# Optimization experiments

Hardware: AMD Instinct MI355X
Metric: run time of the kernel (lower is better)

The kernel has to match this reference:

```python
import jax, jax.numpy as jnp
import numpy as np

B, HP, WP = 4, 32, 32
T = HP * WP
C = 768            # n_embd
NH = 24            # n_head
HS = C // NH       # head_size == HEAD_SIZE == 32
E = HS             # TIME_MIX_EXTRA_DIM = HEAD_SIZE
D = 64             # TIME_DECAY_DIM


def setup_inputs() -> dict:
    key = jax.random.key(0)
    ks = jax.random.split(key, 24)
    small = lambda k, sh: jax.random.uniform(k, sh, jnp.float32, -1e-4, 1e-4)
    inp = {
        "x": jax.random.normal(ks[0], (B, T, C), jnp.float32),
        "time_maa_x": jax.random.uniform(ks[1], (1, 1, C), jnp.float32),
        "time_maa_w": jax.random.uniform(ks[2], (1, 1, C), jnp.float32),
        "time_maa_k": jax.random.uniform(ks[3], (1, 1, C), jnp.float32),
        "time_maa_v": jax.random.uniform(ks[4], (1, 1, C), jnp.float32),
        "time_maa_r": jax.random.uniform(ks[5], (1, 1, C), jnp.float32),
        "time_maa_g": jax.random.uniform(ks[6], (1, 1, C), jnp.float32),
        "time_maa_w1": small(ks[7], (C, 5 * E)),
        "time_maa_w2": small(ks[8], (5, E, C)),
        "time_decay": jnp.linspace(-6.0, -1.0, C, dtype=jnp.float32).reshape(1, 1, C),
        "time_decay_w1": small(ks[9], (C, D)),
        "time_decay_w2": small(ks[10], (D, C)),
        "time_faaaa": jax.random.uniform(ks[11], (NH, HS), jnp.float32, -0.1, 0.6),
        "W_r": jax.random.normal(ks[12], (C, C), jnp.float32) * 0.02,
        "W_k": jax.random.normal(ks[13], (C, C), jnp.float32) * 0.02,
        "W_v": jax.random.normal(ks[14], (C, C), jnp.float32) * 0.02,
        "W_g": jax.random.normal(ks[15], (C, C), jnp.float32) * 0.02,
        "W_o": jax.random.normal(ks[16], (C, C), jnp.float32) * 0.02,
        "ln_w": jnp.ones((C,), jnp.float32),
        "ln_b": jnp.zeros((C,), jnp.float32),
        "Hp": HP,
        "Wp": WP,
    }
    return inp


def q_shift(x, H, W):
    """groups_q_shift with K=1, gamma=1/4: quarter-channel 4-direction spatial shift, zero-padded."""
    Bs, Ts, Cs = x.shape
    g = x.reshape(Bs, H, W, Cs)
    c4 = Cs // 4
    a, b, c, d = g[..., :c4], g[..., c4:2 * c4], g[..., 2 * c4:3 * c4], g[..., 3 * c4:]
    a = jnp.pad(a[:, :, :-1], ((0, 0), (0, 0), (1, 0), (0, 0)))  # shift +W (right)
    b = jnp.pad(b[:, :, 1:], ((0, 0), (0, 0), (0, 1), (0, 0)))   # shift -W (left)
    c = jnp.pad(c[:, :-1], ((0, 0), (1, 0), (0, 0), (0, 0)))     # shift +H (down)
    d = jnp.pad(d[:, 1:], ((0, 0), (0, 1), (0, 0), (0, 0)))      # shift -H (up)
    return jnp.concatenate([a, b, c, d], axis=-1).reshape(Bs, Ts, Cs)


def wkv6(r, k, v, w, u):
    """RWKV6 WKV scan. r,k,v,w: (B,T,C); u: (NH,HS). decay = exp(-exp(w))."""
    Bs, Ts, Cs = r.shape
    rh = r.reshape(Bs, Ts, NH, HS)
    kh = k.reshape(Bs, Ts, NH, HS)
    vh = v.reshape(Bs, Ts, NH, HS)
    dh = jnp.exp(-jnp.exp(w)).reshape(Bs, Ts, NH, HS)

    def step(s, ins):
        rt, kt, vt, dt = ins                                   # each (B,NH,HS)
        kv = kt[..., :, None] * vt[..., None, :]               # (B,NH,HS,HS)
        y = jnp.einsum('bhj,bhji->bhi', rt, s + u[None, :, :, None] * kv)
        s = dt[..., :, None] * s + kv
        return s, y

    xs = (rh.transpose(1, 0, 2, 3), kh.transpose(1, 0, 2, 3),
          vh.transpose(1, 0, 2, 3), dh.transpose(1, 0, 2, 3))
    s0 = jnp.zeros((Bs, NH, HS, HS), r.dtype)
    _, ys = jax.lax.scan(step, s0, xs)                          # (T,B,NH,HS)
    return ys.transpose(1, 0, 2, 3).reshape(Bs, Ts, Cs)


def reference(x, time_maa_x, time_maa_w, time_maa_k, time_maa_v, time_maa_r,
              time_maa_g, time_maa_w1, time_maa_w2, time_decay, time_decay_w1,
              time_decay_w2, time_faaaa, W_r, W_k, W_v, W_g, W_o, ln_w, ln_b,
              Hp, Wp):
    Bs, Ts, Cs = x.shape
    xx = q_shift(x, Hp, Wp) - x                                 # token shift delta
    xxx = x + xx * time_maa_x
    xxx = jnp.tanh(xxx @ time_maa_w1).reshape(Bs, Ts, 5, E)
    mix = jnp.einsum('btke,kec->kbtc', xxx, time_maa_w2)        # (5,B,T,C)
    mw, mk, mv, mr, mg = mix[0], mix[1], mix[2], mix[3], mix[4]

    xw = x + xx * (time_maa_w + mw)
    xk = x + xx * (time_maa_k + mk)
    xv = x + xx * (time_maa_v + mv)
    xr = x + xx * (time_maa_r + mr)
    xg = x + xx * (time_maa_g + mg)

    r = xr @ W_r
    k = xk @ W_k
    v = xv @ W_v
    g = jax.nn.silu(xg @ W_g)

    ww = jnp.tanh(xw @ time_decay_w1) @ time_decay_w2
    w = time_decay + ww                                         # data-dependent log-decay

    y = wkv6(r, k, v, w, time_faaaa)

    # ln_x (LayerNorm over channels)
    mu = y.mean(-1, keepdims=True)
    var = ((y - mu) ** 2).mean(-1, keepdims=True)
    yn = (y - mu) / jnp.sqrt(var + 1e-5) * ln_w + ln_b

    return (yn * g) @ W_o
```

## Files before the change

### kernel.cpp

```cpp
#include <hip/hip_runtime.h>
#include <math.h>

#define BB   4
#define TT   1024
#define CC   768
#define NH_  24
#define HS_  32

static constexpr size_t SZ = (size_t)BB * TT * CC;

typedef __attribute__((ext_vector_type(8))) __bf16 bf16x8;
typedef __attribute__((ext_vector_type(4))) float  f32x4;

__device__ __forceinline__ unsigned short f2bf(float f) {
    unsigned u = __float_as_uint(f);
    unsigned r = (u + 0x7FFFu + ((u >> 16) & 1u)) >> 16;
    return (unsigned short)r;
}
__device__ __forceinline__ float bf2f(unsigned short h) {
    return __uint_as_float(((unsigned)h) << 16);
}

struct TDesc { const float* src; unsigned short* dst; int R, C; };
struct TArgs { TDesc d[8]; };

__global__ __launch_bounds__(256) void transpose_cast(TArgs a)
{
    __shared__ float tile[32][33];
    TDesc t = a.d[blockIdx.z];
    const int tx0 = blockIdx.x * 32, ty0 = blockIdx.y * 32;
    if (tx0 >= t.C || ty0 >= t.R) return;
    const int tx = threadIdx.x & 31, ty = threadIdx.x >> 5;
    #pragma unroll
    for (int dy = 0; dy < 4; ++dy) {
        int rr = ty0 + ty + dy * 8, cc = tx0 + tx;
        tile[ty + dy * 8][tx] = (rr < t.R && cc < t.C) ? t.src[(size_t)rr * t.C + cc] : 0.f;
    }
    __syncthreads();
    #pragma unroll
    for (int dy = 0; dy < 4; ++dy) {
        int cc = tx0 + ty + dy * 8, rr = ty0 + tx;
        if (cc < t.C && rr < t.R)
            t.dst[(size_t)cc * t.R + rr] = f2bf(tile[tx][ty + dy * 8]);
    }
}

__global__ __launch_bounds__(192) void w2fill(const float* __restrict__ w2,
                                              unsigned short* __restrict__ W2t)
{
    const int n = blockIdx.x;
    const int e = threadIdx.x;
    if (e >= 160) return;
    const int kk = n / 768;
    const int c  = n - kk * 768;
    unsigned short val = 0;
    if ((e >> 5) == kk) val = f2bf(w2[(size_t)e * 768 + c]);
    W2t[(size_t)n * 160 + e] = val;
}

__global__ __launch_bounds__(256) void shift_kernel(
    const float* __restrict__ x, const float* __restrict__ maa_x,
    float* __restrict__ xxO, unsigned short* __restrict__ xxxO)
{
    const int tok = blockIdx.x;
    const int t   = tok & (TT - 1);
    const int hh  = t >> 5;
    const int wp  = t & 31;
    const int tid = threadIdx.x;
    const float* xrow = x + (size_t)tok * CC;
    for (int c = tid; c < CC; c += 256) {
        float xc = xrow[c];
        float sh;
        if (c < 192)      sh = (wp > 0)  ? xrow[c - CC]      : 0.f;
        else if (c < 384) sh = (wp < 31) ? xrow[c + CC]      : 0.f;
        else if (c < 576) sh = (hh > 0)  ? xrow[c - 32 * CC] : 0.f;
        else              sh = (hh < 31) ? xrow[c + 32 * CC] : 0.f;
        float xxv = sh - xc;
        size_t o = (size_t)tok * CC + c;
        xxO[o]  = xxv;
        xxxO[o] = f2bf(fmaf(xxv, maa_x[c], xc));
    }
}

template<int KDIM, class Epi>
__device__ __forceinline__ void gemm_core(const unsigned short* __restrict__ A,
                                          const unsigned short* __restrict__ W,
                                          int N, const Epi& epi)
{
    __shared__ __align__(16) unsigned short As[64][40];
    __shared__ __align__(16) unsigned short Bs[64][40];

    const int tid  = threadIdx.x;
    const int lane = tid & 63;
    const int wv   = tid >> 6;
    const int wm   = (wv >> 1) * 32, wn = (wv & 1) * 32;
    const int m0   = blockIdx.y * 64, n0 = blockIdx.x * 64;
    const int srow = tid >> 2, scb = (tid & 3) * 8;
    const int l15  = lane & 15, kb8 = (lane >> 4) * 8;

    f32x4 acc[2][2];
    #pragma unroll
    for (int a = 0; a < 2; ++a)
        #pragma unroll
        for (int b = 0; b < 2; ++b)
            #pragma unroll
            for (int e = 0; e < 4; ++e) acc[a][b][e] = 0.f;

    const unsigned short* aP = A + (size_t)(m0 + srow) * KDIM + scb;
    const unsigned short* bP = W + (size_t)(n0 + srow) * KDIM + scb;
    const bool bvalid = (n0 + srow) < N;

    for (int k0 = 0; k0 < KDIM; k0 += 32) {
        uint4 av = *(const uint4*)(aP + k0);
        uint4 bw = make_uint4(0u, 0u, 0u, 0u);
        if (bvalid) bw = *(const uint4*)(bP + k0);
        *(uint4*)&As[srow][scb] = av;
        *(uint4*)&Bs[srow][scb] = bw;
        __syncthreads();

        bf16x8 a0 = *(const bf16x8*)&As[wm + l15][kb8];
        bf16x8 a1 = *(const bf16x8*)&As[wm + 16 + l15][kb8];
        bf16x8 b0 = *(const bf16x8*)&Bs[wn + l15][kb8];
        bf16x8 b1 = *(const bf16x8*)&Bs[wn + 16 + l15][kb8];
        acc[0][0] = __builtin_amdgcn_mfma_f32_16x16x32_bf16(a0, b0, acc[0][0], 0, 0, 0);
        acc[0][1] = __builtin_amdgcn_mfma_f32_16x16x32_bf16(a0, b1, acc[0][1], 0, 0, 0);
        acc[1][0] = __builtin_amdgcn_mfma_f32_16x16x32_bf16(a1, b0, acc[1][0], 0, 0, 0);
        acc[1][1] = __builtin_amdgcn_mfma_f32_16x16x32_bf16(a1, b1, acc[1][1], 0, 0, 0);
        __syncthreads();
    }

    const int rb_ = m0 + wm + (lane >> 4) * 4;
    #pragma unroll
    for (int mi = 0; mi < 2; ++mi)
        #pragma unroll
        for (int ni = 0; ni < 2; ++ni) {
            int col = n0 + wn + ni * 16 + l15;
            if (col < N) {
                #pragma unroll
                for (int j = 0; j < 4; ++j)
                    epi(rb_ + mi * 16 + j, col, acc[mi][ni][j]);
            }
        }
}

struct EpiTanh {
    unsigned short* O; int ldo;
    __device__ void operator()(int r, int c, float v) const {
        O[(size_t)r * ldo + c] = f2bf(tanhf(v));
    }
};
struct EpiF32 {
    float* O;
    __device__ void operator()(int r, int c, float v) const {
        O[(size_t)r * 768 + c] = v;
    }
};
struct EpiDec {
    const float* td; float* O;
    __device__ void operator()(int r, int c, float v) const {
        O[(size_t)r * 768 + c] = expf(-expf(td[c] + v));
    }
};
struct EpiMix {
    const float* px; const float* pxx;
    const float* maa[5];
    unsigned short* outs[5];
    __device__ void operator()(int r, int c, float v) const {
        int kk = c / 768;
        int cc = c - kk * 768;
        size_t o = (size_t)r * 768 + cc;
        outs[kk][o] = f2bf(fmaf(pxx[o], maa[kk][cc] + v, px[o]));
    }
};
struct EpiRKVG {
    unsigned short* O; bool silu;
    __device__ void operator()(int r, int c, float v) const {
        if (silu) v = v / (1.f + expf(-v));
        O[(size_t)r * 768 + c] = f2bf(v);
    }
};

template<int KDIM, class Epi>
__global__ __launch_bounds__(256) void gemm_one(const unsigned short* __restrict__ A,
                                                const unsigned short* __restrict__ W,
                                                int N, Epi epi)
{
    gemm_core<KDIM>(A, W, N, epi);
}

struct QuadArgs {
    const unsigned short* A[4];
    const unsigned short* W[4];
    unsigned short* O[4];
};
__global__ __launch_bounds__(256) void gemm_quad768(QuadArgs q)
{
    const int z = blockIdx.z;
    EpiRKVG e{q.O[z], z == 3};
    gemm_core<768>(q.A[z], q.W[z], 768, e);
}

__global__ __launch_bounds__(256) void wkv_scan(
    const unsigned short* __restrict__ r, const unsigned short* __restrict__ k,
    const unsigned short* __restrict__ v, const float* __restrict__ dec,
    const float* __restrict__ u, float* __restrict__ y)
{
    __shared__ __align__(16) unsigned short rwL[64][40], kwL[64][40];
    __shared__ __align__(16) unsigned short vT0[32][40], vT1[32][40];
    __shared__ __align__(16) unsigned short rsL[64][40], ksL[64][40];
    __shared__ __align__(16) unsigned short ksT0[32][40], ksT1[32][40];
    __shared__ __align__(16) unsigned short PL0[64][40], PL1[64][40];
    __shared__ __align__(16) unsigned short STb[32][40];
    __shared__ float ST[32][32];
    __shared__ float AL[65][32];
    __shared__ float segprod[8][32];
    __shared__ float dpart[64][4];
    __shared__ float diagL[64];
    __shared__ float uL[32];

    const int bh = blockIdx.x;
    const int b = bh / NH_, h = bh % NH_;
    const int tid  = threadIdx.x;
    const int lane = tid & 63;
    const int wv   = tid >> 6;
    const int l15  = lane & 15;
    const int kb8  = (lane >> 4) * 8;
    const int rb4  = (lane >> 4) * 4;

    const size_t base0 = ((size_t)b * TT) * CC + (size_t)h * HS_;

    if (tid < 32) uL[tid] = u[h * HS_ + tid];
    for (int q = tid; q < 1024; q += 256) {
        ST[q >> 5][q & 31]  = 0.f;
        STb[q >> 5][q & 31] = 0;
    }
    __syncthreads();

    const int lrow = tid >> 2, lq = (tid & 3) * 8;
    const int cj = tid & 31, cseg = tid >> 5;

    for (int tc = 0; tc < TT; tc += 64) {
        {
            size_t gp = base0 + (size_t)(tc + lrow) * CC + lq;
            uint4 rv = *(const uint4*)(r + gp);
            uint4 kv = *(const uint4*)(k + gp);
            uint4 vv = *(const uint4*)(v + gp);
            *(uint4*)&rwL[lrow][lq] = rv;
            *(uint4*)&kwL[lrow][lq] = kv;
            const unsigned short* vp = (const unsigned short*)&vv;
            if (lrow < 32) {
                #pragma unroll
                for (int e = 0; e < 8; ++e) vT0[lq + e][lrow] = vp[e];
            } else {
                #pragma unroll
                for (int e = 0; e < 8; ++e) vT1[lq + e][lrow - 32] = vp[e];
            }
        }
        float dv[8];
        #pragma unroll
        for (int q = 0; q < 8; ++q)
            dv[q] = dec[base0 + (size_t)(tc + cseg * 8 + q) * CC + cj];
        {
            float lp = dv[0];
            #pragma unroll
            for (int q = 1; q < 8; ++q) lp *= dv[q];
            segprod[cseg][cj] = lp;
        }
        __syncthreads();

        {
            const int ptau = tid >> 2, pp = tid & 3;
            float acc = 0.f;
            #pragma unroll
            for (int e = 0; e < 8; ++e) {
                int j = pp * 8 + e;
                acc += bf2f(rwL[ptau][j]) * uL[j] * bf2f(kwL[ptau][j]);
            }
            dpart[ptau][pp] = acc;
        }
        {
            float pre = 1.f;
            #pragma unroll
            for (int s = 0; s < 7; ++s) if (s < cseg) pre *= segprod[s][cj];
            float run = pre;
            #pragma unroll
            for (int q = 0; q < 8; ++q) {
                AL[cseg * 8 + q][cj] = run;
                run *= dv[q];
            }
            if (cseg == 7) AL[64][cj] = run;
        }
        __syncthreads();

        if (tid < 64)
            diagL[tid] = dpart[tid][0] + dpart[tid][1] + dpart[tid][2] + dpart[tid][3];

        #pragma unroll
        for (int q = 0; q < 8; ++q) {
            int tau = cseg * 8 + q;
            float a  = AL[tau][cj];
            float ia = 1.f / AL[tau + 1][cj];
            unsigned short rs = f2bf(bf2f(rwL[tau][cj]) * a);
            unsigned short ks = f2bf(bf2f(kwL[tau][cj]) * ia);
            rsL[tau][cj] = rs;
            ksL[tau][cj] = ks;
            if (tau < 32) ksT0[cj][tau] = ks; else ksT1[cj][tau - 32] = ks;
        }
        __syncthreads();

        {
            const int wm = (wv >> 1) * 32, wn = (wv & 1) * 32;
            bf16x8 a0 = *(const bf16x8*)&rsL[wm + l15][kb8];
            bf16x8 a1 = *(const bf16x8*)&rsL[wm + 16 + l15][kb8];
            bf16x8 b0 = *(const bf16x8*)&ksL[wn + l15][kb8];
            bf16x8 b1 = *(const bf16x8*)&ksL[wn + 16 + l15][kb8];
            f32x4 qf[2][2];
            #pragma unroll
            for (int mi = 0; mi < 2; ++mi)
                #pragma unroll
                for (int ni = 0; ni < 2; ++ni)
                    #pragma unroll
                    for (int e = 0; e < 4; ++e) qf[mi][ni][e] = 0.f;
            qf[0][0] = __builtin_amdgcn_mfma_f32_16x16x32_bf16(a0, b0, qf[0][0], 0, 0, 0);
            qf[0][1] = __builtin_amdgcn_mfma_f32_16x16x32_bf16(a0, b1, qf[0][1], 0, 0, 0);
            qf[1][0] = __builtin_amdgcn_mfma_f32_16x16x32_bf16(a1, b0, qf[1][0], 0, 0, 0);
            qf[1][1] = __builtin_amdgcn_mfma_f32_16x16x32_bf16(a1, b1, qf[1][1], 0, 0, 0);
            #pragma unroll
            for (int mi = 0; mi < 2; ++mi)
                #pragma unroll
                for (int ni = 0; ni < 2; ++ni) {
                    const int col = wn + ni * 16 + l15;
                    #pragma unroll
                    for (int jj = 0; jj < 4; ++jj) {
                        const int row = wm + mi * 16 + rb4 + jj;
                        float val = (col < row) ? qf[mi][ni][jj]
                                  : ((col == row) ? diagL[row] : 0.f);
                        unsigned short bvv = f2bf(val);
                        if (col < 32) PL0[row][col] = bvv;
                        else          PL1[row][col - 32] = bvv;
                    }
                }
        }
        __syncthreads();

        {
            const int mr = wv * 16;
            bf16x8 pa0 = *(const bf16x8*)&PL0[mr + l15][kb8];
            bf16x8 pa1 = *(const bf16x8*)&PL1[mr + l15][kb8];
            bf16x8 ra  = *(const bf16x8*)&rsL[mr + l15][kb8];
            #pragma unroll
            for (int ni = 0; ni < 2; ++ni) {
                bf16x8 bv0 = *(const bf16x8*)&vT0[ni * 16 + l15][kb8];
                bf16x8 bv1 = *(const bf16x8*)&vT1[ni * 16 + l15][kb8];
                bf16x8 bs  = *(const bf16x8*)&STb[ni * 16 + l15][kb8];
                f32x4 acc;
                #pragma unroll
                for (int e = 0; e < 4; ++e) acc[e] = 0.f;
                acc = __builtin_amdgcn_mfma_f32_16x16x32_bf16(pa0, bv0, acc, 0, 0, 0);
                acc = __builtin_amdgcn_mfma_f32_16x16x32_bf16(pa1, bv1, acc, 0, 0, 0);
                acc = __builtin_amdgcn_mfma_f32_16x16x32_bf16(ra,  bs,  acc, 0, 0, 0);
                #pragma unroll
                for (int jj = 0; jj < 4; ++jj)
                    y[base0 + (size_t)(tc + mr + rb4 + jj) * CC + ni * 16 + l15] = acc[jj];
            }
        }
        __syncthreads();

        {
            const int mi = (wv >> 1) * 16, nj = (wv & 1) * 16;
            bf16x8 av0 = *(const bf16x8*)&vT0[mi + l15][kb8];
            bf16x8 av1 = *(const bf16x8*)&vT1[mi + l15][kb8];
            bf16x8 bk0 = *(const bf16x8*)&ksT0[nj + l15][kb8];
            bf16x8 bk1 = *(const bf16x8*)&ksT1[nj + l15][kb8];
            f32x4 acc;
            #pragma unroll
            for (int e = 0; e < 4; ++e) acc[e] = 0.f;
            acc = __builtin_amdgcn_mfma_f32_16x16x32_bf16(av0, bk0, acc, 0, 0, 0);
            acc = __builtin_amdgcn_mfma_f32_16x16x32_bf16(av1, bk1, acc, 0, 0, 0);
            const int j = nj + l15;
            const float D = AL[64][j];
            #pragma unroll
            for (int jj = 0; jj < 4; ++jj) {
                const int i = mi + rb4 + jj;
                float ns = D * (ST[i][j] + acc[jj]);
                ST[i][j]  = ns;
                STb[i][j] = f2bf(ns);
            }
        }
        __syncthreads();
    }
}

__global__ __launch_bounds__(256) void ln_gate(
    const float* __restrict__ y, const unsigned short* __restrict__ g,
    const float* __restrict__ lnw, const float* __restrict__ lnb,
    unsigned short* __restrict__ z)
{
    __shared__ float sy[CC];
    __shared__ float rbuf[8];
    __shared__ float stats[2];

    const int row = blockIdx.x, tid = threadIdx.x;
    const float* yr = y + (size_t)row * CC;

    float s1 = 0.f, s2 = 0.f;
    #pragma unroll
    for (int q = 0; q < 3; ++q) {
        int c = tid + q * 256;
        float vv = yr[c];
        sy[c] = vv;
        s1 += vv;
        s2 += vv * vv;
    }
    #pragma unroll
    for (int off = 32; off > 0; off >>= 1) {
        s1 += __shfl_down(s1, off);
        s2 += __shfl_down(s2, off);
    }
    const int wid = tid >> 6;
    if ((tid & 63) == 0) { rbuf[wid] = s1; rbuf[4 + wid] = s2; }
    __syncthreads();
    if (tid == 0) {
        float S1 = rbuf[0] + rbuf[1] + rbuf[2] + rbuf[3];
        float S2 = rbuf[4] + rbuf[5] + rbuf[6] + rbuf[7];
        float mu = S1 / (float)CC;
        float var = S2 / (float)CC - mu * mu;
        stats[0] = mu;
        stats[1] = rsqrtf(var + 1e-5f);
    }
    __syncthreads();
    const float mu = stats[0], rstd = stats[1];
    const unsigned short* gr = g + (size_t)row * CC;
    unsigned short* zr = z + (size_t)row * CC;
    #pragma unroll
    for (int q = 0; q < 3; ++q) {
        int c = tid + q * 256;
        zr[c] = f2bf(fmaf((sy[c] - mu) * rstd, lnw[c], lnb[c]) * bf2f(gr[c]));
    }
}

extern "C" void kernel_launch(void* const* d_in, const int* in_sizes, int n_in,
                              void* d_out, int out_size, void* d_ws, size_t ws_size,
                              hipStream_t stream)
{
    const float* x      = (const float*)d_in[0];
    const float* maa_x  = (const float*)d_in[1];
    const float* maa_w  = (const float*)d_in[2];
    const float* maa_k  = (const float*)d_in[3];
    const float* maa_v  = (const float*)d_in[4];
    const float* maa_r  = (const float*)d_in[5];
    const float* maa_g  = (const float*)d_in[6];
    const float* w1     = (const float*)d_in[7];
    const float* w2     = (const float*)d_in[8];
    const float* tdec   = (const float*)d_in[9];
    const float* tdw1   = (const float*)d_in[10];
    const float* tdw2   = (const float*)d_in[11];
    const float* faaaa  = (const float*)d_in[12];
    const float* Wr     = (const float*)d_in[13];
    const float* Wk     = (const float*)d_in[14];
    const float* Wv     = (const float*)d_in[15];
    const float* Wg     = (const float*)d_in[16];
    const float* Wo     = (const float*)d_in[17];
    const float* lnw    = (const float*)d_in[18];
    const float* lnb    = (const float*)d_in[19];

    char* base = (char*)d_ws;
    size_t off = 0;
    auto alloc = [&](size_t bytes) -> char* {
        char* p = base + off;
        off = (off + bytes + 255) & ~(size_t)255;
        return p;
    };

    float*          xx   = (float*)alloc(SZ * 4);
    float*          decb = (float*)alloc(SZ * 4);
    unsigned short* xxx  = (unsigned short*)alloc(SZ * 2);
    unsigned short* xw   = (unsigned short*)alloc(SZ * 2);
    unsigned short* xk   = (unsigned short*)alloc(SZ * 2);
    unsigned short* xv   = (unsigned short*)alloc(SZ * 2);
    unsigned short* xr   = (unsigned short*)alloc(SZ * 2);
    unsigned short* xg   = (unsigned short*)alloc(SZ * 2);
    unsigned short* rb   = (unsigned short*)alloc(SZ * 2);
    unsigned short* kb   = (unsigned short*)alloc(SZ * 2);
    unsigned short* vb   = (unsigned short*)alloc(SZ * 2);
    unsigned short* gb   = (unsigned short*)alloc(SZ * 2);
    unsigned short* t5   = (unsigned short*)alloc((size_t)4096 * 160 * 2);
    unsigned short* d1   = (unsigned short*)alloc((size_t)4096 * 64 * 2);
    unsigned short* w1t  = (unsigned short*)alloc((size_t)160 * 768 * 2);
    unsigned short* w2t  = (unsigned short*)alloc((size_t)3840 * 160 * 2);
    unsigned short* wrt  = (unsigned short*)alloc((size_t)768 * 768 * 2);
    unsigned short* wkt  = (unsigned short*)alloc((size_t)768 * 768 * 2);
    unsigned short* wvt  = (unsigned short*)alloc((size_t)768 * 768 * 2);
    unsigned short* wgt  = (unsigned short*)alloc((size_t)768 * 768 * 2);
    unsigned short* wot  = (unsigned short*)alloc((size_t)768 * 768 * 2);
    unsigned short* td1t = (unsigned short*)alloc((size_t)64 * 768 * 2);
    unsigned short* td2t = (unsigned short*)alloc((size_t)768 * 64 * 2);
    float*          y    = xx;
    unsigned short* z    = xxx;

    TArgs ta = {{
        { w1,   w1t,  768, 160 },
        { Wr,   wrt,  768, 768 },
        { Wk,   wkt,  768, 768 },
        { Wv,   wvt,  768, 768 },
        { Wg,   wgt,  768, 768 },
        { Wo,   wot,  768, 768 },
        { tdw1, td1t, 768, 64  },
        { tdw2, td2t, 64,  768 },
    }};
    transpose_cast<<<dim3(24, 24, 8), 256, 0, stream>>>(ta);
    w2fill<<<3840, 192, 0, stream>>>(w2, w2t);

    shift_kernel<<<BB * TT, 256, 0, stream>>>(x, maa_x, xx, xxx);

    gemm_one<768, EpiTanh><<<dim3(3, 64), 256, 0, stream>>>(xxx, w1t, 160, EpiTanh{t5, 160});

    EpiMix em{ x, xx,
               { maa_w, maa_k, maa_v, maa_r, maa_g },
               { xw, xk, xv, xr, xg } };
    gemm_one<160, EpiMix><<<dim3(60, 64), 256, 0, stream>>>(t5, w2t, 3840, em);

    gemm_one<768, EpiTanh><<<dim3(1, 64), 256, 0, stream>>>(xw, td1t, 64, EpiTanh{d1, 64});

    gemm_one<64, EpiDec><<<dim3(12, 64), 256, 0, stream>>>(d1, td2t, 768, EpiDec{tdec, decb});

    QuadArgs qa = {{ xr, xk, xv, xg }, { wrt, wkt, wvt, wgt }, { rb, kb, vb, gb }};
    gemm_quad768<<<dim3(12, 64, 4), 256, 0, stream>>>(qa);

    wkv_scan<<<BB * NH_, 256, 0, stream>>>(rb, kb, vb, decb, faaaa, y);

    ln_gate<<<BB * TT, 256, 0, stream>>>(y, gb, lnw, lnb, z);

    gemm_one<768, EpiF32><<<dim3(12, 64), 256, 0, stream>>>(z, wot, 768, EpiF32{(float*)d_out});
}
```

Baseline: 321.7 us.

## Split WKV scan into chunk-parallel local/carry/state-add kernels; use 128x128 GEMM tiles

The sequential per-head WKV scan, which used only 96 blocks, is split into three kernels. The first computes each 64-token chunk's intra-chunk output and chunk kv outer product in parallel (16 chunks × 96 heads). The second is a short serial carry of the state across chunks, and the third adds the r·state contribution per chunk. Separately, the mix, RKVG quad and output GEMMs move to a new 128x128 tile core with more MFMA work per LDS load. This adds extra kernel launches and global round trips for the intermediates, reuses scratch buffers, and cuts block counts for the GEMMs.

After: 302.7 us. 1.06x faster.

```diff
diff --git a/kernel.cpp b/kernel.cpp
--- a/kernel.cpp
+++ b/kernel.cpp
@@ -6,6 +6,9 @@
 #define CC   768
 #define NH_  24
 #define HS_  32
+#define NBH  (BB * NH_)
+#define NCH  16
+#define CL   64
 
 static constexpr size_t SZ = (size_t)BB * TT * CC;
 
@@ -143,6 +146,78 @@
         }
 }
 
+template<int KDIM, class Epi>
+__device__ __forceinline__ void gemm_core128(const unsigned short* __restrict__ A,
+                                             const unsigned short* __restrict__ W,
+                                             int N, const Epi& epi)
+{
+    __shared__ __align__(16) unsigned short As[128][40];
+    __shared__ __align__(16) unsigned short Bs[128][40];
+
+    const int tid  = threadIdx.x;
+    const int lane = tid & 63;
+    const int wv   = tid >> 6;
+    const int wm   = (wv >> 1) * 64, wn = (wv & 1) * 64;
+    const int m0   = blockIdx.y * 128, n0 = blockIdx.x * 128;
+    const int l15  = lane & 15, kb8 = (lane >> 4) * 8, rb4 = (lane >> 4) * 4;
+    const int sr   = tid >> 2, sq = (tid & 3) * 8;
+
+    f32x4 acc[4][4];
+    #pragma unroll
+    for (int a = 0; a < 4; ++a)
+        #pragma unroll
+        for (int b = 0; b < 4; ++b)
+            #pragma unroll
+            for (int e = 0; e < 4; ++e) acc[a][b][e] = 0.f;
+
+    const unsigned short* aP  = A + (size_t)(m0 + sr) * KDIM + sq;
+    const unsigned short* aP2 = aP + (size_t)64 * KDIM;
+    const unsigned short* bP  = W + (size_t)(n0 + sr) * KDIM + sq;
+    const unsigned short* bP2 = bP + (size_t)64 * KDIM;
+    const bool bv1 = (n0 + sr) < N, bv2 = (n0 + 64 + sr) < N;
+
+    for (int k0 = 0; k0 < KDIM; k0 += 32) {
+        uint4 a1 = *(const uint4*)(aP + k0);
+        uint4 a2 = *(const uint4*)(aP2 + k0);
+        uint4 b1 = make_uint4(0u, 0u, 0u, 0u);
+        uint4 b2 = make_uint4(0u, 0u, 0u, 0u);
+        if (bv1) b1 = *(const uint4*)(bP + k0);
+        if (bv2) b2 = *(const uint4*)(bP2 + k0);
+        *(uint4*)&As[sr][sq]      = a1;
+        *(uint4*)&As[64 + sr][sq] = a2;
+        *(uint4*)&Bs[sr][sq]      = b1;
+        *(uint4*)&Bs[64 + sr][sq] = b2;
+        __syncthreads();
+
+        bf16x8 af[4], bfr[4];
+        #pragma unroll
+        for (int mi = 0; mi < 4; ++mi)
+            af[mi] = *(const bf16x8*)&As[wm + mi * 16 + l15][kb8];
+        #pragma unroll
+        for (int ni = 0; ni < 4; ++ni)
+            bfr[ni] = *(const bf16x8*)&Bs[wn + ni * 16 + l15][kb8];
+        #pragma unroll
+        for (int mi = 0; mi < 4; ++mi)
+            #pragma unroll
+            for (int ni = 0; ni < 4; ++ni)
+                acc[mi][ni] = __builtin_amdgcn_mfma_f32_16x16x32_bf16(af[mi], bfr[ni], acc[mi][ni], 0, 0, 0);
+        __syncthreads();
+    }
+
+    const int rbase = m0 + wm + rb4;
+    #pragma unroll
+    for (int mi = 0; mi < 4; ++mi)
+        #pragma unroll
+        for (int ni = 0; ni < 4; ++ni) {
+            int col = n0 + wn + ni * 16 + l15;
+            if (col < N) {
+                #pragma unroll
+                for (int j = 0; j < 4; ++j)
+                    epi(rbase + mi * 16 + j, col, acc[mi][ni][j]);
+            }
+        }
+}
+
 struct EpiTanh {
     unsigned short* O; int ldo;
     __device__ void operator()(int r, int c, float v) const {
@@ -188,6 +263,14 @@
     gemm_core<KDIM>(A, W, N, epi);
 }
 
+template<int KDIM, class Epi>
+__global__ __launch_bounds__(256) void gemm_one128(const unsigned short* __restrict__ A,
+                                                   const unsigned short* __restrict__ W,
+                                                   int N, Epi epi)
+{
+    gemm_core128<KDIM>(A, W, N, epi);
+}
+
 struct QuadArgs {
     const unsigned short* A[4];
     const unsigned short* W[4];
@@ -197,28 +280,28 @@
 {
     const int z = blockIdx.z;
     EpiRKVG e{q.O[z], z == 3};
-    gemm_core<768>(q.A[z], q.W[z], 768, e);
-}
-
-__global__ __launch_bounds__(256) void wkv_scan(
+    gemm_core128<768>(q.A[z], q.W[z], 768, e);
+}
+
+__global__ __launch_bounds__(256) void wkv_local(
     const unsigned short* __restrict__ r, const unsigned short* __restrict__ k,
     const unsigned short* __restrict__ v, const float* __restrict__ dec,
-    const float* __restrict__ u, float* __restrict__ y)
+    const float* __restrict__ u, float* __restrict__ y,
+    unsigned short* __restrict__ rsb, float* __restrict__ kvt,
+    float* __restrict__ dcv)
 {
     __shared__ __align__(16) unsigned short rwL[64][40], kwL[64][40];
     __shared__ __align__(16) unsigned short vT0[32][40], vT1[32][40];
-    __shared__ __align__(16) unsigned short rsL[64][40], ksL[64][40];
     __shared__ __align__(16) unsigned short ksT0[32][40], ksT1[32][40];
     __shared__ __align__(16) unsigned short PL0[64][40], PL1[64][40];
-    __shared__ __align__(16) unsigned short STb[32][40];
-    __shared__ float ST[32][32];
     __shared__ float AL[65][32];
     __shared__ float segprod[8][32];
     __shared__ float dpart[64][4];
     __shared__ float diagL[64];
     __shared__ float uL[32];
 
-    const int bh = blockIdx.x;
+    const int c   = blockIdx.x;
+    const int bh  = blockIdx.y;
     const int b = bh / NH_, h = bh % NH_;
     const int tid  = threadIdx.x;
     const int lane = tid & 63;
@@ -226,168 +309,224 @@
     const int l15  = lane & 15;
     const int kb8  = (lane >> 4) * 8;
     const int rb4  = (lane >> 4) * 4;
+    const int tc   = c * CL;
 
     const size_t base0 = ((size_t)b * TT) * CC + (size_t)h * HS_;
 
     if (tid < 32) uL[tid] = u[h * HS_ + tid];
-    for (int q = tid; q < 1024; q += 256) {
-        ST[q >> 5][q & 31]  = 0.f;
-        STb[q >> 5][q & 31] = 0;
-    }
-    __syncthreads();
 
     const int lrow = tid >> 2, lq = (tid & 3) * 8;
     const int cj = tid & 31, cseg = tid >> 5;
 
-    for (int tc = 0; tc < TT; tc += 64) {
-        {
-            size_t gp = base0 + (size_t)(tc + lrow) * CC + lq;
-            uint4 rv = *(const uint4*)(r + gp);
-            uint4 kv = *(const uint4*)(k + gp);
-            uint4 vv = *(const uint4*)(v + gp);
-            *(uint4*)&rwL[lrow][lq] = rv;
-            *(uint4*)&kwL[lrow][lq] = kv;
-            const unsigned short* vp = (const unsigned short*)&vv;
-            if (lrow < 32) {
+    {
+        size_t gp = base0 + (size_t)(tc + lrow) * CC + lq;
+        uint4 rv = *(const uint4*)(r + gp);
+        uint4 kv = *(const uint4*)(k + gp);
+        uint4 vv = *(const uint4*)(v + gp);
+        *(uint4*)&rwL[lrow][lq] = rv;
+        *(uint4*)&kwL[lrow][lq] = kv;
+        const unsigned short* vp = (const unsigned short*)&vv;
+        if (lrow < 32) {
+            #pragma unroll
+            for (int e = 0; e < 8; ++e) vT0[lq + e][lrow] = vp[e];
+        } else {
+            #pragma unroll
+            for (int e = 0; e < 8; ++e) vT1[lq + e][lrow - 32] = vp[e];
+        }
+    }
+    float dv[8];
+    #pragma unroll
+    for (int q = 0; q < 8; ++q)
+        dv[q] = dec[base0 + (size_t)(tc + cseg * 8 + q) * CC + cj];
+    {
+        float lp = dv[0];
+        #pragma unroll
+        for (int q = 1; q < 8; ++q) lp *= dv[q];
+        segprod[cseg][cj] = lp;
+    }
+    __syncthreads();
+
+    {
+        const int ptau = tid >> 2, pp = tid & 3;
+        float acc = 0.f;
+        #pragma unroll
+        for (int e = 0; e < 8; ++e) {
+            int j = pp * 8 + e;
+            acc += bf2f(rwL[ptau][j]) * uL[j] * bf2f(kwL[ptau][j]);
+        }
+        dpart[ptau][pp] = acc;
+    }
+    {
+        float pre = 1.f;
+        #pragma unroll
+        for (int s = 0; s < 7; ++s) if (s < cseg) pre *= segprod[s][cj];
+        float run = pre;
+        #pragma unroll
+        for (int q = 0; q < 8; ++q) {
+            AL[cseg * 8 + q][cj] = run;
+            run *= dv[q];
+        }
+        if (cseg == 7) AL[64][cj] = run;
+    }
+    __syncthreads();
+
+    if (tid < 64)
+        diagL[tid] = dpart[tid][0] + dpart[tid][1] + dpart[tid][2] + dpart[tid][3];
+    if (tid < 32)
+        dcv[((size_t)bh * NCH + c) * 32 + tid] = AL[64][tid];
+
+    #pragma unroll
+    for (int q = 0; q < 8; ++q) {
+        int tau = cseg * 8 + q;
+        float a  = AL[tau][cj];
+        float ia = 1.f / AL[tau + 1][cj];
+        unsigned short rs = f2bf(bf2f(rwL[tau][cj]) * a);
+        unsigned short ks = f2bf(bf2f(kwL[tau][cj]) * ia);
+        rwL[tau][cj] = rs;
+        kwL[tau][cj] = ks;
+        if (tau < 32) ksT0[cj][tau] = ks; else ksT1[cj][tau - 32] = ks;
+    }
+    __syncthreads();
+
+    {
+        const int wm = (wv >> 1) * 32, wn = (wv & 1) * 32;
+        bf16x8 a0 = *(const bf16x8*)&rwL[wm + l15][kb8];
+        bf16x8 a1 = *(const bf16x8*)&rwL[wm + 16 + l15][kb8];
+        bf16x8 b0 = *(const bf16x8*)&kwL[wn + l15][kb8];
+        bf16x8 b1 = *(const bf16x8*)&kwL[wn + 16 + l15][kb8];
+        f32x4 qf[2][2];
+        #pragma unroll
+        for (int mi = 0; mi < 2; ++mi)
+            #pragma unroll
+            for (int ni = 0; ni < 2; ++ni)
                 #pragma unroll
-                for (int e = 0; e < 8; ++e) vT0[lq + e][lrow] = vp[e];
-            } else {
+                for (int e = 0; e < 4; ++e) qf[mi][ni][e] = 0.f;
+        qf[0][0] = __builtin_amdgcn_mfma_f32_16x16x32_bf16(a0, b0, qf[0][0], 0, 0, 0);
+        qf[0][1] = __builtin_amdgcn_mfma_f32_16x16x32_bf16(a0, b1, qf[0][1], 0, 0, 0);
+        qf[1][0] = __builtin_amdgcn_mfma_f32_16x16x32_bf16(a1, b0, qf[1][0], 0, 0, 0);
+        qf[1][1] = __builtin_amdgcn_mfma_f32_16x16x32_bf16(a1, b1, qf[1][1], 0, 0, 0);
+        #pragma unroll
+        for (int mi = 0; mi < 2; ++mi)
+            #pragma unroll
+            for (int ni = 0; ni < 2; ++ni) {
+                const int col = wn + ni * 16 + l15;
                 #pragma unroll
-                for (int e = 0; e < 8; ++e) vT1[lq + e][lrow - 32] = vp[e];
+                for (int jj = 0; jj < 4; ++jj) {
+                    const int row = wm + mi * 16 + rb4 + jj;
+                    float val = (col < row) ? qf[mi][ni][jj]
+                              : ((col == row) ? diagL[row] : 0.f);
+                    unsigned short bvv = f2bf(val);
+                    if (col < 32) PL0[row][col] = bvv;
+                    else          PL1[row][col - 32] = bvv;
+                }
             }
-        }
-        float dv[8];
-        #pragma unroll
-        for (int q = 0; q < 8; ++q)
-            dv[q] = dec[base0 + (size_t)(tc + cseg * 8 + q) * CC + cj];
-        {
-            float lp = dv[0];
-            #pragma unroll
-            for (int q = 1; q < 8; ++q) lp *= dv[q];
-            segprod[cseg][cj] = lp;
-        }
-        __syncthreads();
-
-        {
-            const int ptau = tid >> 2, pp = tid & 3;
-            float acc = 0.f;
-            #pragma unroll
-            for (int e = 0; e < 8; ++e) {
-                int j = pp * 8 + e;
-                acc += bf2f(rwL[ptau][j]) * uL[j] * bf2f(kwL[ptau][j]);
-            }
-            dpart[ptau][pp] = acc;
-        }
-        {
-            float pre = 1.f;
-            #pragma unroll
-            for (int s = 0; s < 7; ++s) if (s < cseg) pre *= segprod[s][cj];
-            float run = pre;
-            #pragma unroll
-            for (int q = 0; q < 8; ++q) {
-                AL[cseg * 8 + q][cj] = run;
-                run *= dv[q];
-            }
-            if (cseg == 7) AL[64][cj] = run;
-        }
-        __syncthreads();
-
-        if (tid < 64)
-            diagL[tid] = dpart[tid][0] + dpart[tid][1] + dpart[tid][2] + dpart[tid][3];
-
-        #pragma unroll
-        for (int q = 0; q < 8; ++q) {
-            int tau = cseg * 8 + q;
-            float a  = AL[tau][cj];
-            float ia = 1.f / AL[tau + 1][cj];
-            unsigned short rs = f2bf(bf2f(rwL[tau][cj]) * a);
-            unsigned short ks = f2bf(bf2f(kwL[tau][cj]) * ia);
-            rsL[tau][cj] = rs;
-            ksL[tau][cj] = ks;
-            if (tau < 32) ksT0[cj][tau] = ks; else ksT1[cj][tau - 32] = ks;
-        }
-        __syncthreads();
-
-        {
-            const int wm = (wv >> 1) * 32, wn = (wv & 1) * 32;
-            bf16x8 a0 = *(const bf16x8*)&rsL[wm + l15][kb8];
-            bf16x8 a1 = *(const bf16x8*)&rsL[wm + 16 + l15][kb8];
-            bf16x8 b0 = *(const bf16x8*)&ksL[wn + l15][kb8];
-            bf16x8 b1 = *(const bf16x8*)&ksL[wn + 16 + l15][kb8];
-            f32x4 qf[2][2];
-            #pragma unroll
-            for (int mi = 0; mi < 2; ++mi)
-                #pragma unroll
-                for (int ni = 0; ni < 2; ++ni)
-                    #pragma unroll
-                    for (int e = 0; e < 4; ++e) qf[mi][ni][e] = 0.f;
-            qf[0][0] = __builtin_amdgcn_mfma_f32_16x16x32_bf16(a0, b0, qf[0][0], 0, 0, 0);
-            qf[0][1] = __builtin_amdgcn_mfma_f32_16x16x32_bf16(a0, b1, qf[0][1], 0, 0, 0);
-            qf[1][0] = __builtin_amdgcn_mfma_f32_16x16x32_bf16(a1, b0, qf[1][0], 0, 0, 0);
-            qf[1][1] = __builtin_amdgcn_mfma_f32_16x16x32_bf16(a1, b1, qf[1][1], 0, 0, 0);
-            #pragma unroll
-            for (int mi = 0; mi < 2; ++mi)
-                #pragma unroll
-                for (int ni = 0; ni < 2; ++ni) {
-                    const int col = wn + ni * 16 + l15;
-                    #pragma unroll
-                    for (int jj = 0; jj < 4; ++jj) {
-                        const int row = wm + mi * 16 + rb4 + jj;
-                        float val = (col < row) ? qf[mi][ni][jj]
-                                  : ((col == row) ? diagL[row] : 0.f);
-                        unsigned short bvv = f2bf(val);
-                        if (col < 32) PL0[row][col] = bvv;
-                        else          PL1[row][col - 32] = bvv;
-                    }
-                }
-        }
-        __syncthreads();
-
-        {
-            const int mr = wv * 16;
-            bf16x8 pa0 = *(const bf16x8*)&PL0[mr + l15][kb8];
-            bf16x8 pa1 = *(const bf16x8*)&PL1[mr + l15][kb8];
-            bf16x8 ra  = *(const bf16x8*)&rsL[mr + l15][kb8];
-            #pragma unroll
-            for (int ni = 0; ni < 2; ++ni) {
-                bf16x8 bv0 = *(const bf16x8*)&vT0[ni * 16 + l15][kb8];
-                bf16x8 bv1 = *(const bf16x8*)&vT1[ni * 16 + l15][kb8];
-                bf16x8 bs  = *(const bf16x8*)&STb[ni * 16 + l15][kb8];
-                f32x4 acc;
-                #pragma unroll
-                for (int e = 0; e < 4; ++e) acc[e] = 0.f;
-                acc = __builtin_amdgcn_mfma_f32_16x16x32_bf16(pa0, bv0, acc, 0, 0, 0);
-                acc = __builtin_amdgcn_mfma_f32_16x16x32_bf16(pa1, bv1, acc, 0, 0, 0);
-                acc = __builtin_amdgcn_mfma_f32_16x16x32_bf16(ra,  bs,  acc, 0, 0, 0);
-                #pragma unroll
-                for (int jj = 0; jj < 4; ++jj)
-                    y[base0 + (size_t)(tc + mr + rb4 + jj) * CC + ni * 16 + l15] = acc[jj];
-            }
-        }
-        __syncthreads();
-
-        {
-            const int mi = (wv >> 1) * 16, nj = (wv & 1) * 16;
-            bf16x8 av0 = *(const bf16x8*)&vT0[mi + l15][kb8];
-            bf16x8 av1 = *(const bf16x8*)&vT1[mi + l15][kb8];
-            bf16x8 bk0 = *(const bf16x8*)&ksT0[nj + l15][kb8];
-            bf16x8 bk1 = *(const bf16x8*)&ksT1[nj + l15][kb8];
+    }
+    __syncthreads();
+
+    *(uint4*)(rsb + base0 + (size_t)(tc + lrow) * CC + lq) = *(const uint4*)&rwL[lrow][lq];
+
+    {
+        const int mr = wv * 16;
+        bf16x8 pa0 = *(const bf16x8*)&PL0[mr + l15][kb8];
+        bf16x8 pa1 = *(const bf16x8*)&PL1[mr + l15][kb8];
+        #pragma unroll
+        for (int ni = 0; ni < 2; ++ni) {
+            bf16x8 bv0 = *(const bf16x8*)&vT0[ni * 16 + l15][kb8];
+            bf16x8 bv1 = *(const bf16x8*)&vT1[ni * 16 + l15][kb8];
             f32x4 acc;
             #pragma unroll
             for (int e = 0; e < 4; ++e) acc[e] = 0.f;
-            acc = __builtin_amdgcn_mfma_f32_16x16x32_bf16(av0, bk0, acc, 0, 0, 0);
-            acc = __builtin_amdgcn_mfma_f32_16x16x32_bf16(av1, bk1, acc, 0, 0, 0);
-            const int j = nj + l15;
-            const float D = AL[64][j];
-            #pragma unroll
-            for (int jj = 0; jj < 4; ++jj) {
-                const int i = mi + rb4 + jj;
-                float ns = D * (ST[i][j] + acc[jj]);
-                ST[i][j]  = ns;
-                STb[i][j] = f2bf(ns);
-            }
-        }
-        __syncthreads();
+            acc = __builtin_amdgcn_mfma_f32_16x16x32_bf16(pa0, bv0, acc, 0, 0, 0);
+            acc = __builtin_amdgcn_mfma_f32_16x16x32_bf16(pa1, bv1, acc, 0, 0, 0);
+            #pragma unroll
+            for (int jj = 0; jj < 4; ++jj)
+                y[base0 + (size_t)(tc + mr + rb4 + jj) * CC + ni * 16 + l15] = acc[jj];
+        }
+    }
+
+    {
+        const int mi_ = (wv >> 1) * 16, nj = (wv & 1) * 16;
+        bf16x8 av0 = *(const bf16x8*)&vT0[mi_ + l15][kb8];
+        bf16x8 av1 = *(const bf16x8*)&vT1[mi_ + l15][kb8];
+        bf16x8 bk0 = *(const bf16x8*)&ksT0[nj + l15][kb8];
+        bf16x8 bk1 = *(const bf16x8*)&ksT1[nj + l15][kb8];
+        f32x4 acc;
+        #pragma unroll
+        for (int e = 0; e < 4; ++e) acc[e] = 0.f;
+        acc = __builtin_amdgcn_mfma_f32_16x16x32_bf16(av0, bk0, acc, 0, 0, 0);
+        acc = __builtin_amdgcn_mfma_f32_16x16x32_bf16(av1, bk1, acc, 0, 0, 0);
+        const int j = nj + l15;
+        const size_t sb = ((size_t)bh * NCH + c) << 10;
+        #pragma unroll
+        for (int jj = 0; jj < 4; ++jj)
+            kvt[sb + (size_t)(mi_ + rb4 + jj) * 32 + j] = acc[jj];
+    }
+}
+
+__global__ __launch_bounds__(256) void wkv_carry(
+    const float* __restrict__ kvt, const float* __restrict__ dcv,
+    unsigned short* __restrict__ spv)
+{
+    const int bh = blockIdx.x;
+    const int tid = threadIdx.x;
+    const int e0 = tid << 2;
+    const int j0 = e0 & 31;
+    float s0 = 0.f, s1 = 0.f, s2 = 0.f, s3 = 0.f;
+    #pragma unroll
+    for (int c = 0; c < NCH; ++c) {
+        const size_t sb = (size_t)bh * NCH + c;
+        float4 kv = *(const float4*)(kvt + (sb << 10) + e0);
+        float4 d4 = *(const float4*)(dcv + sb * 32 + j0);
+        s0 = d4.x * (s0 + kv.x);
+        s1 = d4.y * (s1 + kv.y);
+        s2 = d4.z * (s2 + kv.z);
+        s3 = d4.w * (s3 + kv.w);
+        if (c < NCH - 1) {
+            unsigned lo = (unsigned)f2bf(s0) | ((unsigned)f2bf(s1) << 16);
+            unsigned hi = (unsigned)f2bf(s2) | ((unsigned)f2bf(s3) << 16);
+            *(uint2*)(spv + ((sb + 1) << 10) + e0) = make_uint2(lo, hi);
+        }
+    }
+}
+
+__global__ __launch_bounds__(256) void wkv_stadd(
+    const unsigned short* __restrict__ rsb, const unsigned short* __restrict__ spv,
+    float* __restrict__ y)
+{
+    __shared__ __align__(16) unsigned short rsL[64][40];
+    __shared__ __align__(16) unsigned short STb[32][40];
+
+    const int c  = blockIdx.x + 1;
+    const int bh = blockIdx.y;
+    const int b = bh / NH_, h = bh % NH_;
+    const int tid = threadIdx.x, lane = tid & 63, wv = tid >> 6;
+    const int l15 = lane & 15, kb8 = (lane >> 4) * 8, rb4 = (lane >> 4) * 4;
+    const int tc = c * CL;
+    const size_t base0 = ((size_t)b * TT) * CC + (size_t)h * HS_;
+    const int lrow = tid >> 2, lq = (tid & 3) * 8;
+
+    *(uint4*)&rsL[lrow][lq] = *(const uint4*)(rsb + base0 + (size_t)(tc + lrow) * CC + lq);
+    if (tid < 128) {
+        int row = tid >> 2, q = (tid & 3) * 8;
+        *(uint4*)&STb[row][q] =
+            *(const uint4*)(spv + (((size_t)bh * NCH + c) << 10) + (size_t)row * 32 + q);
+    }
+    __syncthreads();
+
+    const int mr = wv * 16;
+    bf16x8 ra = *(const bf16x8*)&rsL[mr + l15][kb8];
+    #pragma unroll
+    for (int ni = 0; ni < 2; ++ni) {
+        bf16x8 bs = *(const bf16x8*)&STb[ni * 16 + l15][kb8];
+        f32x4 acc;
+        #pragma unroll
+        for (int e = 0; e < 4; ++e) acc[e] = 0.f;
+        acc = __builtin_amdgcn_mfma_f32_16x16x32_bf16(ra, bs, acc, 0, 0, 0);
+        #pragma unroll
+        for (int jj = 0; jj < 4; ++jj) {
+            size_t gp = base0 + (size_t)(tc + mr + rb4 + jj) * CC + ni * 16 + l15;
+            y[gp] += acc[jj];
+        }
     }
 }
 
@@ -495,8 +634,13 @@
     unsigned short* wot  = (unsigned short*)alloc((size_t)768 * 768 * 2);
     unsigned short* td1t = (unsigned short*)alloc((size_t)64 * 768 * 2);
     unsigned short* td2t = (unsigned short*)alloc((size_t)768 * 64 * 2);
+
     float*          y    = xx;
     unsigned short* z    = xxx;
+    unsigned short* rsb  = xr;
+    float*          kvtb = (float*)xk;
+    unsigned short* spvb = xv;
+    float*          dcb  = (float*)xg;
 
     TArgs ta = {{
         { w1,   w1t,  768, 160 },
@@ -518,18 +662,20 @@
     EpiMix em{ x, xx,
                { maa_w, maa_k, maa_v, maa_r, maa_g },
                { xw, xk, xv, xr, xg } };
-    gemm_one<160, EpiMix><<<dim3(60, 64), 256, 0, stream>>>(t5, w2t, 3840, em);
+    gemm_one128<160, EpiMix><<<dim3(30, 32), 256, 0, stream>>>(t5, w2t, 3840, em);
 
     gemm_one<768, EpiTanh><<<dim3(1, 64), 256, 0, stream>>>(xw, td1t, 64, EpiTanh{d1, 64});
 
     gemm_one<64, EpiDec><<<dim3(12, 64), 256, 0, stream>>>(d1, td2t, 768, EpiDec{tdec, decb});
 
     QuadArgs qa = {{ xr, xk, xv, xg }, { wrt, wkt, wvt, wgt }, { rb, kb, vb, gb }};
-    gemm_quad768<<<dim3(12, 64, 4), 256, 0, stream>>>(qa);
-
-    wkv_scan<<<BB * NH_, 256, 0, stream>>>(rb, kb, vb, decb, faaaa, y);
+    gemm_quad768<<<dim3(6, 32, 4), 256, 0, stream>>>(qa);
+
+    wkv_local<<<dim3(NCH, NBH), 256, 0, stream>>>(rb, kb, vb, decb, faaaa, y, rsb, kvtb, dcb);
+    wkv_carry<<<NBH, 256, 0, stream>>>(kvtb, dcb, spvb);
+    wkv_stadd<<<dim3(NCH - 1, NBH), 256, 0, stream>>>(rsb, spvb, y);
 
     ln_gate<<<BB * TT, 256, 0, stream>>>(y, gb, lnw, lnb, z);
 
-    gemm_one<768, EpiF32><<<dim3(12, 64), 256, 0, stream>>>(z, wot, 768, EpiF32{(float*)d_out});
-}
+    gemm_one128<768, EpiF32><<<dim3(6, 32), 256, 0, stream>>>(z, wot, 768, EpiF32{(float*)d_out});
+}
```
